# Performance work log

Hardware: AMD Instinct MI355X
Metric: run time of the kernel (lower is better)

## Reference

```python
import jax, jax.numpy as jnp
import numpy as np
from jax.scipy.special import logsumexp

NUM_CLASSES = 2
THRESHOLD = 0.35      # overlap_thresh
NEGPOS_RATIO = 7      # neg_pos
VAR0, VAR1 = 0.1, 0.2  # self.variance


def point_form(p):
    # (cx,cy,w,h) -> (x1,y1,x2,y2)
    return jnp.concatenate([p[:, :2] - p[:, 2:] / 2, p[:, :2] + p[:, 2:] / 2], axis=1)


def jaccard(a, b):
    # a: [T,4] xyxy, b: [P,4] xyxy -> IoU [T,P]
    lt = jnp.maximum(a[:, None, :2], b[None, :, :2])
    rb = jnp.minimum(a[:, None, 2:], b[None, :, 2:])
    wh = jnp.clip(rb - lt, 0.0)
    inter = wh[..., 0] * wh[..., 1]
    area_a = ((a[:, 2] - a[:, 0]) * (a[:, 3] - a[:, 1]))[:, None]
    area_b = ((b[:, 2] - b[:, 0]) * (b[:, 3] - b[:, 1]))[None, :]
    return inter / (area_a + area_b - inter)


def encode(matched, priors):
    # matched xyxy [P,4], priors cxcywh [P,4]
    g_cxcy = ((matched[:, :2] + matched[:, 2:]) / 2 - priors[:, :2]) / (VAR0 * priors[:, 2:])
    g_wh = jnp.log((matched[:, 2:] - matched[:, :2]) / priors[:, 2:]) / VAR1
    return jnp.concatenate([g_cxcy, g_wh], axis=1)


def encode_landm(matched, priors):
    m = matched.reshape(-1, 5, 2)  # [P,5,2]
    g = (m - priors[:, None, :2]) / (VAR0 * priors[:, None, 2:])
    return g.reshape(-1, 10)


def match_one(truths, labels, landms, priors):
    # truths [T,4] xyxy, labels [T], landms [T,10], priors [P,4] cxcywh
    overlaps = jaccard(truths, point_form(priors))  # [T,P]
    best_prior_overlap = overlaps.max(axis=1)       # [T]
    best_prior_idx = overlaps.argmax(axis=1)        # [T]
    valid_gt = best_prior_overlap >= 0.2            # hard-gt filter
    best_truth_overlap = overlaps.max(axis=0)       # [P]
    best_truth_idx = overlaps.argmax(axis=0)        # [P]
    # index_fill_(0, best_prior_idx[valid], 2): IoU <= 1 so scatter-max is exact
    best_truth_overlap = best_truth_overlap.at[best_prior_idx].max(
        jnp.where(valid_gt, 2.0, 0.0))
    best_truth_idx = best_truth_idx.at[best_prior_idx].set(jnp.arange(truths.shape[0]))
    matches = truths[best_truth_idx]                # [P,4]
    conf = jnp.where(best_truth_overlap < THRESHOLD, 0.0, labels[best_truth_idx])
    loc = encode(matches, priors)
    landm = encode_landm(landms[best_truth_idx], priors)
    any_valid = valid_gt.any()                      # early-return branch in torch match()
    loc = jnp.where(any_valid, loc, 0.0)
    conf = jnp.where(any_valid, conf, 0.0)
    landm = jnp.where(any_valid, landm, 0.0)
    return loc, conf.astype(jnp.int32), landm


def smooth_l1(x):
    ax = jnp.abs(x)
    return jnp.where(ax < 1.0, 0.5 * ax * ax, ax - 0.5)


def multibox_loss(loc_data, conf_data, landm_data, priors, targets):
    num_priors = priors.shape[0]
    # torch uses .data (detached) for matching/encoding targets
    truths = jax.lax.stop_gradient(targets[..., :4])
    landms_gt = jax.lax.stop_gradient(targets[..., 4:14])
    labels = jax.lax.stop_gradient(targets[..., 14])
    pri = jax.lax.stop_gradient(priors)
    loc_t, conf_t, landm_t = jax.vmap(match_one, in_axes=(0, 0, 0, None))(
        truths, labels, landms_gt, pri)  # [B,P,4], [B,P], [B,P,10]

    # landmark loss over conf_t > 0
    pos1 = conf_t > 0
    N1 = jnp.maximum(pos1.sum().astype(jnp.float32), 1.0)
    loss_landm = jnp.sum(smooth_l1(landm_data - landm_t) * pos1[..., None])

    # localization loss over conf_t != 0; conf_t[pos] = 1
    pos = conf_t != 0
    conf_t = jnp.where(pos, 1, conf_t)
    loss_l = jnp.sum(smooth_l1(loc_data - loc_t) * pos[..., None])

    # per-prior CE = logsumexp(logits) - logit[target]
    ce = logsumexp(conf_data, axis=-1) - jnp.take_along_axis(
        conf_data, conf_t[..., None], axis=-1)[..., 0]  # [B,P]
    # hard negative mining: zero positives, double-argsort rank trick
    rank_loss = jnp.where(pos, 0.0, ce)
    idx_rank = jnp.argsort(jnp.argsort(-rank_loss, axis=1), axis=1)
    num_pos = pos.sum(axis=1, keepdims=True)
    num_neg = jnp.minimum(NEGPOS_RATIO * num_pos, num_priors - 1)
    neg = idx_rank < num_neg
    loss_c = jnp.sum(jnp.where(pos | neg, ce, 0.0))

    N = jnp.maximum(num_pos.sum().astype(jnp.float32), 1.0)
    return loss_l / N, loss_c / N, loss_landm / N1


def setup_inputs() -> dict:
    key = jax.random.key(0)
    ks = jax.random.split(key, 8)
    B, P, T = 16, 32768, 64
    loc_data = jax.random.normal(ks[0], (B, P, 4), jnp.float32)
    conf_data = jax.random.normal(ks[1], (B, P, NUM_CLASSES), jnp.float32)
    landm_data = jax.random.normal(ks[2], (B, P, 10), jnp.float32)
    # priors: (cx,cy,w,h), all positive and in (0,1)
    cxcy = jax.random.uniform(ks[3], (P, 2), minval=0.05, maxval=0.95)
    wh = jax.random.uniform(ks[4], (P, 2), minval=0.02, maxval=0.3)
    priors = jnp.concatenate([cxcy, wh], axis=1)
    # targets: [x1,y1,x2,y2, 10 landmark coords, label]
    c = jax.random.uniform(ks[5], (B, T, 2), minval=0.15, maxval=0.85)
    s = jax.random.uniform(ks[6], (B, T, 2), minval=0.05, maxval=0.25)
    boxes = jnp.concatenate([c - s / 2, c + s / 2], axis=-1)
    lm = jax.random.uniform(ks[7], (B, T, 10))
    labels = jnp.ones((B, T, 1), jnp.float32)
    targets = jnp.concatenate([boxes, lm, labels], axis=-1)
    return {"loc_data": loc_data, "conf_data": conf_data,
            "landm_data": landm_data, "priors": priors, "targets": targets}


def reference(loc_data, conf_data, landm_data, priors, targets):
    return multibox_loss(loc_data, conf_data, landm_data, priors, targets)
```

## Files before the change

### kernel.cpp

```cpp
#include <hip/hip_runtime.h>
#include <math.h>

#define OVERLAP_THRESH 0.35f
#define VALID_THRESH   0.2f
#define NEGPOS         7
#define TMAX           64
#define NCHUNK         16
#define TPW            4
#define EPT            4
#define HB             2048
#define NC             4
#define NSCAN          32

__device__ __forceinline__ float sl1(float x) {
    float ax = fabsf(x);
    return ax < 1.0f ? 0.5f * ax * ax : ax - 0.5f;
}
__device__ __forceinline__ float frcp(float x) { return __builtin_amdgcn_rcpf(x); }

__device__ __forceinline__ void atomicMaxU8(unsigned char* addr, unsigned char val) {
    size_t a = (size_t)addr;
    unsigned* word = (unsigned*)(a & ~(size_t)3);
    int shift = (int)(a & 3) * 8;
    unsigned old = *word, assumed;
    do {
        unsigned cur = (old >> shift) & 0xFFu;
        if (cur >= val) break;
        assumed = old;
        unsigned nw = (old & ~(0xFFu << shift)) | ((unsigned)val << shift);
        old = atomicCAS(word, assumed, nw);
    } while (old != assumed);
}

__global__ void clear_ws_kernel(uint4* __restrict__ p, size_t n16) {
    size_t i = (size_t)blockIdx.x * blockDim.x + threadIdx.x;
    size_t stride = (size_t)gridDim.x * blockDim.x;
    uint4 z = make_uint4(0u, 0u, 0u, 0u);
    for (; i < n16; i += stride) p[i] = z;
}

__device__ __forceinline__ void select_coarse(const int* gh, int K, int lane,
                                              int* s_d1, int* s_r) {
    int base = lane * 32;
    int v[32]; int s = 0;
    #pragma unroll
    for (int j = 0; j < 32; j++) { v[j] = gh[base + j]; s += v[j]; }
    int sfx = s;
    for (int off = 1; off < 64; off <<= 1) {
        int t = __shfl_down(sfx, off);
        if (lane + off < 64) sfx += t;
    }
    int ge = sfx;
    #pragma unroll
    for (int j = 0; j < 32; j++) {
        int gen = ge - v[j];
        if (ge >= K && gen < K) { *s_d1 = base + j; *s_r = K - gen; }
        ge = gen;
    }
}

__global__ void best_prior_partial_kernel(const float* __restrict__ priors,
                                          const float* __restrict__ targets,
                                          int P, int BT,
                                          unsigned long long* __restrict__ keys) {
    int wid  = blockIdx.x * (blockDim.x >> 6) + (threadIdx.x >> 6);
    int lane = threadIdx.x & 63;
    int ng    = (BT + TPW - 1) / TPW;
    int group = wid % ng;
    int chunk = wid / ng;
    int bt0   = group * TPW;

    float tx1[TPW], ty1[TPW], tx2[TPW], ty2[TPW], ta[TPW];
    #pragma unroll
    for (int j = 0; j < TPW; j++) {
        int bt = min(bt0 + j, BT - 1);
        const float* tg = targets + (size_t)bt * 15;
        tx1[j] = tg[0]; ty1[j] = tg[1]; tx2[j] = tg[2]; ty2[j] = tg[3];
        ta[j]  = (tx2[j] - tx1[j]) * (ty2[j] - ty1[j]);
    }

    int cs = (P + NCHUNK - 1) / NCHUNK;
    int p0 = chunk * cs;
    int pend = min(p0 + cs, P);
    float best[TPW]; int bestp[TPW];
    #pragma unroll
    for (int j = 0; j < TPW; j++) { best[j] = -1.0f; bestp[j] = p0; }

    for (int p = p0 + lane; p < pend; p += 64) {
        float4 pr = ((const float4*)priors)[p];
        float hw = pr.z * 0.5f, hh = pr.w * 0.5f;
        float px1 = pr.x - hw, py1 = pr.y - hh;
        float px2 = pr.x + hw, py2 = pr.y + hh;
        float pa = (px2 - px1) * (py2 - py1);
        #pragma unroll
        for (int j = 0; j < TPW; j++) {
            float iw = fmaxf(fminf(tx2[j], px2) - fmaxf(tx1[j], px1), 0.0f);
            float ih = fmaxf(fminf(ty2[j], py2) - fmaxf(ty1[j], py1), 0.0f);
            float inter = iw * ih;
            float iou = inter * frcp(ta[j] + pa - inter);
            if (iou > best[j]) { best[j] = iou; bestp[j] = p; }
        }
    }
    #pragma unroll
    for (int j = 0; j < TPW; j++) {
        unsigned long long key =
            ((unsigned long long)__float_as_uint(fmaxf(best[j], 0.0f)) << 32) |
            (unsigned long long)(0xFFFFFFFFu - (unsigned)bestp[j]);
        for (int off = 32; off; off >>= 1) {
            unsigned long long k2 = __shfl_down(key, off);
            if (k2 > key) key = k2;
        }
        if (lane == 0 && bt0 + j < BT) atomicMax(&keys[bt0 + j], key);
    }
}

__global__ void unpack_override_kernel(const unsigned long long* __restrict__ keys,
                                       int T, int BT, int P,
                                       unsigned char* __restrict__ ovr8,
                                       unsigned* __restrict__ vmask,
                                       int* __restrict__ av_arr) {
    int i = blockIdx.x * blockDim.x + threadIdx.x;
    if (i >= BT) return;
    unsigned long long k = keys[i];
    int bpi = (int)(0xFFFFFFFFu - (unsigned)(k & 0xFFFFFFFFull));
    float iou = __uint_as_float((unsigned)(k >> 32));
    int b = i / T, t = i % T;
    atomicMaxU8(&ovr8[(size_t)b * P + bpi], (unsigned char)(t + 1));
    if (iou >= VALID_THRESH) {
        atomicOr(&vmask[(size_t)b * (P >> 5) + (bpi >> 5)], 1u << (bpi & 31));
        atomicOr(&av_arr[b], 1);
    }
}

__global__ void match_loss_fused_kernel(const float* __restrict__ priors,
                                        const float* __restrict__ targets,
                                        const float* __restrict__ loc_data,
                                        const float* __restrict__ conf_data,
                                        const float* __restrict__ landm_data,
                                        const unsigned char* __restrict__ ovr8,
                                        const unsigned* __restrict__ vmask,
                                        const int* __restrict__ av_arr,
                                        int P, int T,
                                        float* __restrict__ rank_loss,
                                        int* __restrict__ ghist,
                                        int* __restrict__ num_pos,
                                        int* __restrict__ num_pos1,
                                        float* __restrict__ accb)
{
    int b   = blockIdx.y;
    int tid = threadIdx.x;
    int p0  = (blockIdx.x * blockDim.x + tid) * EPT;
    size_t base = (size_t)b * P + p0;

    __shared__ float4 s_box[TMAX];
    __shared__ float  s_ba[TMAX];
    __shared__ float  s_lab[TMAX];
    __shared__ int    s_hist[HB][NC];
    __shared__ float  s_ll, s_llm, s_cep;
    __shared__ int    s_np, s_np1;

    if (tid == 0) { s_ll = 0.f; s_llm = 0.f; s_cep = 0.f; s_np = 0; s_np1 = 0; }
    for (int i = tid; i < HB; i += blockDim.x)
        *(int4*)&s_hist[i][0] = make_int4(0, 0, 0, 0);
    if (tid < T) {
        const float* tg = targets + ((size_t)b * T + tid) * 15;
        float x1 = tg[0], y1 = tg[1], x2 = tg[2], y2 = tg[3];
        s_box[tid] = make_float4(x1, y1, x2, y2);
        s_ba[tid]  = (x2 - x1) * (y2 - y1);
        s_lab[tid] = tg[14];
    }
    __syncthreads();

    int hc = tid & (NC - 1);
    int av = av_arr[b];
    float ll_s = 0.f, cep_s = 0.f, llm_s = 0.f;
    int np_s = 0, np1_s = 0;

    if (p0 + EPT <= P) {
        float px1[EPT], py1[EPT], px2[EPT], py2[EPT], pa[EPT];
        float pcx[EPT], pcy[EPT], pw[EPT], ph[EPT];
        float best[EPT]; int btidx[EPT];
        #pragma unroll
        for (int j = 0; j < EPT; j++) {
            float4 pr = ((const float4*)priors)[p0 + j];
            float hw = pr.z * 0.5f, hh = pr.w * 0.5f;
            px1[j] = pr.x - hw; py1[j] = pr.y - hh;
            px2[j] = pr.x + hw; py2[j] = pr.y + hh;
            pa[j]  = (px2[j] - px1[j]) * (py2[j] - py1[j]);
            pcx[j] = pr.x; pcy[j] = pr.y; pw[j] = pr.z; ph[j] = pr.w;
            best[j] = -1.0f; btidx[j] = 0;
        }

        #pragma unroll 8
        for (int t = 0; t < TMAX; t++) {
            float4 box = s_box[t];
            float  ba  = s_ba[t];
            #pragma unroll
            for (int j = 0; j < EPT; j++) {
                float iw = fmaxf(fminf(box.z, px2[j]) - fmaxf(box.x, px1[j]), 0.0f);
                float ih = fmaxf(fminf(box.w, py2[j]) - fmaxf(box.y, py1[j]), 0.0f);
                float inter = iw * ih;
                float iou = inter * frcp(ba + pa[j] - inter);
                if (iou > best[j]) { best[j] = iou; btidx[j] = t; }
            }
        }

        unsigned ov4 = *(const unsigned*)&ovr8[base];
        unsigned vb  = vmask[(size_t)b * (P >> 5) + (p0 >> 5)] >> (p0 & 31);
        float cc[2 * EPT];
        *(float4*)&cc[0] = ((const float4*)(conf_data + base * 2))[0];
        *(float4*)&cc[4] = ((const float4*)(conf_data + base * 2))[1];

        float rl[EPT]; int btv[EPT]; float cev[EPT]; int posv[EPT];
        #pragma unroll
        for (int j = 0; j < EPT; j++) {
            int bt = btidx[j];
            int ov = (ov4 >> (8 * j)) & 0xFF;
            if (ov) bt = ov - 1;
            float bv = best[j];
            if ((vb >> j) & 1u) bv = 2.0f;
            btv[j] = bt;

            bool cond = (av && bv >= OVERLAP_THRESH);
            float lab = cond ? s_lab[bt] : 0.0f;
            int   ci  = (int)lab;
            bool  pos = cond && (ci != 0);
            posv[j] = pos;

            float c0 = cc[2 * j], c1 = cc[2 * j + 1];
            float mx = fmaxf(c0, c1);
            float lse = mx + __logf(1.0f + __expf(-fabsf(c0 - c1)));
            float ce  = lse - (pos ? c1 : c0);
            cev[j] = ce;
            rl[j] = pos ? 0.0f : fmaxf(ce, 0.0f);
            atomicAdd(&s_hist[__float_as_uint(rl[j]) >> 20][hc], 1);
        }
        *(float4*)&rank_loss[base] = *(float4*)rl;

        #pragma unroll
        for (int j = 0; j < EPT; j++) {
            if (!posv[j]) continue;
            int bt = btv[j];
            size_t idx = base + j;
            float4 mb = s_box[bt];
            bool pos1 = ((int)s_lab[bt] > 0);

            float rx = frcp(0.1f * pw[j]), ry = frcp(0.1f * ph[j]);
            float gx = ((mb.x + mb.z) * 0.5f - pcx[j]) * rx;
            float gy = ((mb.y + mb.w) * 0.5f - pcy[j]) * ry;
            float gw = __logf((mb.z - mb.x) * frcp(pw[j])) * 5.0f;
            float gh = __logf((mb.w - mb.y) * frcp(ph[j])) * 5.0f;
            const float* ld = loc_data + idx * 4;
            ll_s += sl1(ld[0] - gx) + sl1(ld[1] - gy) + sl1(ld[2] - gw) + sl1(ld[3] - gh);
            cep_s += cev[j];
            np_s++;

            if (pos1) {
                const float* lmd = landm_data + idx * 10;
                const float* lm  = targets + ((size_t)b * T + bt) * 15 + 4;
                float s = 0.0f;
                #pragma unroll
                for (int k = 0; k < 5; k++) {
                    float gxl = (lm[2 * k]     - pcx[j]) * rx;
                    float gyl = (lm[2 * k + 1] - pcy[j]) * ry;
                    s += sl1(lmd[2 * k] - gxl) + sl1(lmd[2 * k + 1] - gyl);
                }
                llm_s += s;
                np1_s++;
            }
        }
    }

    if (np_s)  { atomicAdd(&s_ll, ll_s); atomicAdd(&s_cep, cep_s); atomicAdd(&s_np, np_s); }
    if (np1_s) { atomicAdd(&s_llm, llm_s); atomicAdd(&s_np1, np1_s); }
    __syncthreads();
    if (tid == 0) {
        if (s_np)  { atomicAdd(&num_pos[b], s_np);
                     atomicAdd(&accb[b * 3 + 0], s_ll);
                     atomicAdd(&accb[b * 3 + 2], s_cep); }
        if (s_np1) { atomicAdd(&num_pos1[b], s_np1);
                     atomicAdd(&accb[b * 3 + 1], s_llm); }
    }
    for (int i = tid; i < HB; i += blockDim.x) {
        int4 v4 = *(int4*)&s_hist[i][0];
        int v = v4.x + v4.y + v4.z + v4.w;
        if (v) atomicAdd(&ghist[(size_t)b * HB + i], v);
    }
}

__device__ __forceinline__ void select_digit(const int* hist, int nb, int tid,
                                             int* s_dig, int* s_r) {
    if (tid < 64) {
        int lane = tid;
        int per  = (nb >= 64) ? (nb >> 6) : 1;
        int base = lane * per;
        int v[4]; int s = 0;
        #pragma unroll
        for (int j = 0; j < 4; j++) {
            int idx = base + j;
            int h = (j < per && idx < nb) ? hist[idx] : 0;
            v[j] = h; s += h;
        }
        int sfx = s;
        for (int off = 1; off < 64; off <<= 1) {
            int t = __shfl_down(sfx, off);
            if (lane + off < 64) sfx += t;
        }
        int r  = *s_r;
        int ge = sfx;
        #pragma unroll
        for (int j = 0; j < 4; j++) {
            int gen = ge - v[j];
            int d   = base + j;
            if (j < per && d < nb && ge >= r && gen < r) { *s_dig = d; *s_r = r - gen; }
            ge = gen;
        }
    }
}

__global__ void topk_scan_kernel(const float* __restrict__ rank_loss,
                                 const int* __restrict__ num_pos,
                                 const int* __restrict__ ghist,
                                 int P,
                                 float* __restrict__ glist,
                                 int* __restrict__ gcnt,
                                 float* __restrict__ accS,
                                 int* __restrict__ accC) {
    int b    = blockIdx.y;
    int tid  = threadIdx.x;
    int lane = tid & 63;
    int wv   = tid >> 6;
    long long Kll = (long long)num_pos[b] * NEGPOS;
    int K = (Kll > P - 1) ? (P - 1) : (int)Kll;
    if (K <= 0) return;

    __shared__ int   s_d1, s_rdummy;
    __shared__ int   s_lcnt, s_base;
    __shared__ float s_stage[1024];
    __shared__ float s_S[4];
    __shared__ int   s_C[4];

    if (tid == 0) s_lcnt = 0;
    if (wv == 0) select_coarse(ghist + (size_t)b * HB, K, lane, &s_d1, &s_rdummy);
    __syncthreads();
    int d1 = s_d1;
    unsigned hi_lim = ((unsigned)(d1 + 1)) << 20;

    const float4* v4 = (const float4*)(rank_loss + (size_t)b * P);
    int n4  = P >> 2;
    int per = (n4 + NSCAN - 1) / NSCAN;
    int i0  = blockIdx.x * per;
    int i1  = min(i0 + per, n4);

    float S = 0.f; int C = 0;
    if (d1 == 0) {
        for (int i = i0 + tid; i < i1; i += blockDim.x) {
            float4 x = v4[i];
            float xs[4] = {x.x, x.y, x.z, x.w};
            #pragma unroll
            for (int k = 0; k < 4; k++) {
                unsigned u = __float_as_uint(xs[k]);
                if (u >= hi_lim) { S += xs[k]; C++; }
            }
        }
    } else {
        for (int i = i0 + tid; i < i1; i += blockDim.x) {
            float4 x = v4[i];
            float xs[4] = {x.x, x.y, x.z, x.w};
            #pragma unroll
            for (int k = 0; k < 4; k++) {
                unsigned u = __float_as_uint(xs[k]);
                if (u >= hi_lim) { S += xs[k]; C++; }
                bool m = ((u >> 20) == (unsigned)d1);
                unsigned long long mk = __ballot(m);
                if (m) {
                    int leader = __ffsll((long long)mk) - 1;
                    int base = 0;
                    if (lane == leader) base = atomicAdd(&s_lcnt, __popcll(mk));
                    base = __shfl(base, leader);
                    int ofs = __popcll(mk & (((unsigned long long)1 << lane) - 1ull));
                    s_stage[base + ofs] = xs[k];
                }
            }
        }
    }
    for (int off = 32; off; off >>= 1) {
        S += __shfl_down(S, off);
        C += __shfl_down(C, off);
    }
    if (lane == 0) { s_S[wv] = S; s_C[wv] = C; }
    __syncthreads();
    if (tid == 0) {
        float St = 0.f; int Ct = 0;
        for (int i = 0; i < 4; i++) { St += s_S[i]; Ct += s_C[i]; }
        if (Ct) { atomicAdd(&accS[b], St); atomicAdd(&accC[b], Ct); }
        s_base = s_lcnt ? atomicAdd(&gcnt[b], s_lcnt) : 0;
    }
    __syncthreads();
    int lc = s_lcnt, gbase = s_base;
    float* gl = glist + (size_t)b * P;
    for (int i = tid; i < lc; i += blockDim.x) gl[gbase + i] = s_stage[i];
}

__global__ void topk_refine_finalize_kernel(const int* __restrict__ num_pos,
                                            const int* __restrict__ num_pos1,
                                            const float* __restrict__ accb,
                                            const int* __restrict__ ghist,
                                            int P, int B,
                                            const float* __restrict__ glist,
                                            const int* __restrict__ gcnt,
                                            const float* __restrict__ accS,
                                            const int* __restrict__ accC,
                                            float* __restrict__ accn,
                                            int* __restrict__ done_ctr,
                                            float* __restrict__ out) {
    int b    = blockIdx.x;
    int tid  = threadIdx.x;
    int lane = tid & 63;
    int wv   = tid >> 6;
    long long Kll = (long long)num_pos[b] * NEGPOS;
    int K = (Kll > P - 1) ? (P - 1) : (int)Kll;

    __shared__ int   hist[256];
    __shared__ int   s_d1, s_r, s_dig;
    __shared__ float s_S[16];
    __shared__ int   s_C[16];
    __shared__ float s_res;

    if (tid == 0) s_res = 0.0f;
    __syncthreads();

    if (K > 0) {
        if (wv == 0) select_coarse(ghist + (size_t)b * HB, K, lane, &s_d1, &s_r);
        __syncthreads();
        int d1 = s_d1;

        if (d1 == 0) {
            if (tid == 0) s_res = accS[b];
            __syncthreads();
        } else {
            int lc = gcnt[b];
            const float* gl = glist + (size_t)b * P;

            unsigned pmask = 0u, pval = 0u;
            const int shf[3] = {12, 4, 0};
            const int nbk[3] = {256, 256, 16};
            int trips = (lc + blockDim.x - 1) / blockDim.x;
            for (int ps = 0; ps < 3; ps++) {
                int sh = shf[ps]; unsigned wm = (unsigned)(nbk[ps] - 1);
                if (tid < 256) hist[tid] = 0;
                __syncthreads();
                for (int tc = 0; tc < trips; tc++) {
                    int i = tc * blockDim.x + tid;
                    bool ok = (i < lc);
                    unsigned u = ok ? __float_as_uint(gl[i]) : 0u;
                    ok = ok && ((u & pmask) == pval);
                    unsigned d = (u >> sh) & wm;
                    unsigned long long m = __ballot(ok);
                    #pragma unroll
                    for (int bit = 0; bit < 8; bit++) {
                        unsigned long long bb = __ballot((d >> bit) & 1u);
                        m &= ((d >> bit) & 1u) ? bb : ~bb;
                    }
                    if (ok && lane == (__ffsll((long long)m) - 1))
                        atomicAdd(&hist[d], __popcll(m));
                }
                __syncthreads();
                select_digit(hist, nbk[ps], tid, &s_dig, &s_r);
                __syncthreads();
                pval  |= ((unsigned)s_dig) << sh;
                pmask |= wm << sh;
            }
            float tau = __uint_as_float((((unsigned)d1) << 20) | pval);

            float S = 0.f; int C = 0;
            for (int i = tid; i < lc; i += blockDim.x) {
                float x = gl[i];
                if (x > tau) { S += x; C++; }
            }
            for (int off = 32; off; off >>= 1) {
                S += __shfl_down(S, off);
                C += __shfl_down(C, off);
            }
            if (lane == 0) { s_S[wv] = S; s_C[wv] = C; }
            __syncthreads();
            if (tid == 0) {
                float St = accS[b]; int Ct = accC[b];
                int nw = blockDim.x >> 6;
                for (int i = 0; i < nw; i++) { St += s_S[i]; Ct += s_C[i]; }
                s_res = St + (float)(K - Ct) * tau;
            }
            __syncthreads();
        }
    }

    if (tid == 0) {
        accn[b] = s_res;
        __threadfence();
        if (atomicAdd(done_ctr, 1) == B - 1) {
            float cen = 0.f;
            for (int j = 0; j < B; j++) cen += atomicAdd(&accn[j], 0.0f);
            int tp = 0, tp1 = 0;
            float ll = 0.f, llm = 0.f, cep = 0.f;
            for (int j = 0; j < B; j++) {
                tp  += num_pos[j];
                tp1 += num_pos1[j];
                ll  += accb[j * 3 + 0];
                llm += accb[j * 3 + 1];
                cep += accb[j * 3 + 2];
            }
            float N  = fmaxf((float)tp, 1.0f);
            float N1 = fmaxf((float)tp1, 1.0f);
            out[0] = ll / N;
            out[1] = (cep + cen) / N;
            out[2] = llm / N1;
        }
    }
}

extern "C" void kernel_launch(void* const* d_in, const int* in_sizes, int n_in,
                              void* d_out, int out_size, void* d_ws, size_t ws_size,
                              hipStream_t stream) {
    const float* loc_data   = (const float*)d_in[0];
    const float* conf_data  = (const float*)d_in[1];
    const float* landm_data = (const float*)d_in[2];
    const float* priors     = (const float*)d_in[3];
    const float* targets    = (const float*)d_in[4];
    float* out = (float*)d_out;

    int P  = in_sizes[3] / 4;
    int BP = in_sizes[0] / 4;
    int B  = BP / P;
    int T  = in_sizes[4] / (B * 15);
    int BT = B * T;

    char* ws = (char*)d_ws;
    float* rank_loss = (float*)ws;                    size_t off = (size_t)B * P * sizeof(float);
    float* glist     = (float*)(ws + off);            off += (size_t)B * P * sizeof(float);
    unsigned char* ovr8 = (unsigned char*)(ws + off); off += (size_t)B * P;
    unsigned* vmask = (unsigned*)(ws + off); off += (size_t)B * (P >> 5) * sizeof(unsigned);
    int* ghist      = (int*)(ws + off);      off += (size_t)B * HB * sizeof(int);
    unsigned long long* keys = (unsigned long long*)(ws + off); off += (size_t)BT * sizeof(unsigned long long);
    int* av_arr     = (int*)(ws + off);      off += (size_t)B * sizeof(int);
    int* num_pos    = (int*)(ws + off);      off += (size_t)B * sizeof(int);
    int* num_pos1   = (int*)(ws + off);      off += (size_t)B * sizeof(int);
    float* accb     = (float*)(ws + off);    off += (size_t)B * 3 * sizeof(float);
    float* accn     = (float*)(ws + off);    off += (size_t)B * sizeof(float);
    int* gcnt       = (int*)(ws + off);      off += (size_t)B * sizeof(int);
    float* accS     = (float*)(ws + off);    off += (size_t)B * sizeof(float);
    int* accC       = (int*)(ws + off);      off += (size_t)B * sizeof(int);
    int* done_ctr   = (int*)(ws + off);      off += sizeof(int);

    size_t zbytes = (size_t)((char*)(done_ctr + 1) - (char*)ovr8);
    size_t n16 = (zbytes + 15) / 16;
    clear_ws_kernel<<<256, 256, 0, stream>>>((uint4*)ovr8, n16);

    int waves   = NCHUNK * ((BT + TPW - 1) / TPW);
    int blocks2 = (waves + 3) / 4;
    best_prior_partial_kernel<<<blocks2, 256, 0, stream>>>(priors, targets, P, BT, keys);

    unpack_override_kernel<<<(BT + 255) / 256, 256, 0, stream>>>(keys, T, BT, P,
                                                                 ovr8, vmask, av_arr);

    dim3 gm((P + 256 * EPT - 1) / (256 * EPT), B);
    match_loss_fused_kernel<<<gm, 256, 0, stream>>>(priors, targets, loc_data, conf_data,
                                                    landm_data, ovr8, vmask, av_arr, P, T,
                                                    rank_loss, ghist, num_pos, num_pos1, accb);

    dim3 gs(NSCAN, B);
    topk_scan_kernel<<<gs, 256, 0, stream>>>(rank_loss, num_pos, ghist, P,
                                             glist, gcnt, accS, accC);

    topk_refine_finalize_kernel<<<B, 1024, 0, stream>>>(num_pos, num_pos1, accb, ghist,
                                                        P, B, glist, gcnt, accS, accC,
                                                        accn, done_ctr, out);
}
```

Baseline: 104.5 us.

## Fuse best-prior search with override unpack; skip positives in histogram

Replaces the chunked best-prior kernel plus the global 64-bit atomicMax keys buffer and separate unpack kernel with one kernel. Each block now scans all priors for four targets and reduces the result in shared memory, then writes the override, valid mask and any-valid flags directly. This removes one launch and the global atomics. Separately, positive priors are no longer added to the rank-loss histogram, and their count is added back to bin 0 in select_coarse, which cuts shared atomics. The trade-off is that each block now walks the full prior range, so there are fewer blocks with longer loops.

```diff
diff --git a/kernel.cpp b/kernel.cpp
--- a/kernel.cpp
+++ b/kernel.cpp
@@ -5,8 +5,7 @@
 #define VALID_THRESH   0.2f
 #define NEGPOS         7
 #define TMAX           64
-#define NCHUNK         16
-#define TPW            4
+#define TPB2           4
 #define EPT            4
 #define HB             2048
 #define NC             4
@@ -39,12 +38,16 @@
     for (; i < n16; i += stride) p[i] = z;
 }
 
-__device__ __forceinline__ void select_coarse(const int* gh, int K, int lane,
+__device__ __forceinline__ void select_coarse(const int* gh, int K, int lane, int add0,
                                               int* s_d1, int* s_r) {
     int base = lane * 32;
     int v[32]; int s = 0;
     #pragma unroll
-    for (int j = 0; j < 32; j++) { v[j] = gh[base + j]; s += v[j]; }
+    for (int j = 0; j < 32; j++) {
+        int h = gh[base + j];
+        if (base + j == 0) h += add0;
+        v[j] = h; s += h;
+    }
     int sfx = s;
     for (int off = 1; off < 64; off <<= 1) {
         int t = __shfl_down(sfx, off);
@@ -59,41 +62,38 @@
     }
 }
 
-__global__ void best_prior_partial_kernel(const float* __restrict__ priors,
-                                          const float* __restrict__ targets,
-                                          int P, int BT,
-                                          unsigned long long* __restrict__ keys) {
-    int wid  = blockIdx.x * (blockDim.x >> 6) + (threadIdx.x >> 6);
-    int lane = threadIdx.x & 63;
-    int ng    = (BT + TPW - 1) / TPW;
-    int group = wid % ng;
-    int chunk = wid / ng;
-    int bt0   = group * TPW;
-
-    float tx1[TPW], ty1[TPW], tx2[TPW], ty2[TPW], ta[TPW];
+__global__ void best_prior_fused_kernel(const float* __restrict__ priors,
+                                        const float* __restrict__ targets,
+                                        int P, int T, int BT,
+                                        unsigned char* __restrict__ ovr8,
+                                        unsigned* __restrict__ vmask,
+                                        int* __restrict__ av_arr) {
+    int tid  = threadIdx.x;
+    int lane = tid & 63;
+    int wv   = tid >> 6;
+    int bt0  = blockIdx.x * TPB2;
+
+    float tx1[TPB2], ty1[TPB2], tx2[TPB2], ty2[TPB2], ta[TPB2];
     #pragma unroll
-    for (int j = 0; j < TPW; j++) {
+    for (int j = 0; j < TPB2; j++) {
         int bt = min(bt0 + j, BT - 1);
         const float* tg = targets + (size_t)bt * 15;
         tx1[j] = tg[0]; ty1[j] = tg[1]; tx2[j] = tg[2]; ty2[j] = tg[3];
         ta[j]  = (tx2[j] - tx1[j]) * (ty2[j] - ty1[j]);
     }
 
-    int cs = (P + NCHUNK - 1) / NCHUNK;
-    int p0 = chunk * cs;
-    int pend = min(p0 + cs, P);
-    float best[TPW]; int bestp[TPW];
+    float best[TPB2]; int bestp[TPB2];
     #pragma unroll
-    for (int j = 0; j < TPW; j++) { best[j] = -1.0f; bestp[j] = p0; }
-
-    for (int p = p0 + lane; p < pend; p += 64) {
+    for (int j = 0; j < TPB2; j++) { best[j] = -1.0f; bestp[j] = 0; }
+
+    for (int p = tid; p < P; p += 256) {
         float4 pr = ((const float4*)priors)[p];
         float hw = pr.z * 0.5f, hh = pr.w * 0.5f;
         float px1 = pr.x - hw, py1 = pr.y - hh;
         float px2 = pr.x + hw, py2 = pr.y + hh;
         float pa = (px2 - px1) * (py2 - py1);
         #pragma unroll
-        for (int j = 0; j < TPW; j++) {
+        for (int j = 0; j < TPB2; j++) {
             float iw = fmaxf(fminf(tx2[j], px2) - fmaxf(tx1[j], px1), 0.0f);
             float ih = fmaxf(fminf(ty2[j], py2) - fmaxf(ty1[j], py1), 0.0f);
             float inter = iw * ih;
@@ -101,8 +101,10 @@
             if (iou > best[j]) { best[j] = iou; bestp[j] = p; }
         }
     }
+
+    __shared__ unsigned long long s_red[TPB2][4];
     #pragma unroll
-    for (int j = 0; j < TPW; j++) {
+    for (int j = 0; j < TPB2; j++) {
         unsigned long long key =
             ((unsigned long long)__float_as_uint(fmaxf(best[j], 0.0f)) << 32) |
             (unsigned long long)(0xFFFFFFFFu - (unsigned)bestp[j]);
@@ -110,25 +112,24 @@
             unsigned long long k2 = __shfl_down(key, off);
             if (k2 > key) key = k2;
         }
-        if (lane == 0 && bt0 + j < BT) atomicMax(&keys[bt0 + j], key);
-    }
-}
-
-__global__ void unpack_override_kernel(const unsigned long long* __restrict__ keys,
-                                       int T, int BT, int P,
-                                       unsigned char* __restrict__ ovr8,
-                                       unsigned* __restrict__ vmask,
-                                       int* __restrict__ av_arr) {
-    int i = blockIdx.x * blockDim.x + threadIdx.x;
-    if (i >= BT) return;
-    unsigned long long k = keys[i];
-    int bpi = (int)(0xFFFFFFFFu - (unsigned)(k & 0xFFFFFFFFull));
-    float iou = __uint_as_float((unsigned)(k >> 32));
-    int b = i / T, t = i % T;
-    atomicMaxU8(&ovr8[(size_t)b * P + bpi], (unsigned char)(t + 1));
-    if (iou >= VALID_THRESH) {
-        atomicOr(&vmask[(size_t)b * (P >> 5) + (bpi >> 5)], 1u << (bpi & 31));
-        atomicOr(&av_arr[b], 1);
+        if (lane == 0) s_red[j][wv] = key;
+    }
+    __syncthreads();
+    if (tid < TPB2) {
+        unsigned long long k = s_red[tid][0];
+        #pragma unroll
+        for (int w = 1; w < 4; w++) if (s_red[tid][w] > k) k = s_red[tid][w];
+        int bt = bt0 + tid;
+        if (bt < BT) {
+            int bpi = (int)(0xFFFFFFFFu - (unsigned)(k & 0xFFFFFFFFull));
+            float iou = __uint_as_float((unsigned)(k >> 32));
+            int b = bt / T, t = bt % T;
+            atomicMaxU8(&ovr8[(size_t)b * P + bpi], (unsigned char)(t + 1));
+            if (iou >= VALID_THRESH) {
+                atomicOr(&vmask[(size_t)b * (P >> 5) + (bpi >> 5)], 1u << (bpi & 31));
+                atomicOr(&av_arr[b], 1);
+            }
+        }
     }
 }
 
@@ -233,7 +234,7 @@
             float ce  = lse - (pos ? c1 : c0);
             cev[j] = ce;
             rl[j] = pos ? 0.0f : fmaxf(ce, 0.0f);
-            atomicAdd(&s_hist[__float_as_uint(rl[j]) >> 20][hc], 1);
+            if (!pos) atomicAdd(&s_hist[__float_as_uint(rl[j]) >> 20][hc], 1);
         }
         *(float4*)&rank_loss[base] = *(float4*)rl;
 
@@ -330,7 +331,8 @@
     int tid  = threadIdx.x;
     int lane = tid & 63;
     int wv   = tid >> 6;
-    long long Kll = (long long)num_pos[b] * NEGPOS;
+    int np   = num_pos[b];
+    long long Kll = (long long)np * NEGPOS;
     int K = (Kll > P - 1) ? (P - 1) : (int)Kll;
     if (K <= 0) return;
 
@@ -341,7 +343,7 @@
     __shared__ int   s_C[4];
 
     if (tid == 0) s_lcnt = 0;
-    if (wv == 0) select_coarse(ghist + (size_t)b * HB, K, lane, &s_d1, &s_rdummy);
+    if (wv == 0) select_coarse(ghist + (size_t)b * HB, K, lane, np, &s_d1, &s_rdummy);
     __syncthreads();
     int d1 = s_d1;
     unsigned hi_lim = ((unsigned)(d1 + 1)) << 20;
@@ -418,7 +420,8 @@
     int tid  = threadIdx.x;
     int lane = tid & 63;
     int wv   = tid >> 6;
-    long long Kll = (long long)num_pos[b] * NEGPOS;
+    int np   = num_pos[b];
+    long long Kll = (long long)np * NEGPOS;
     int K = (Kll > P - 1) ? (P - 1) : (int)Kll;
 
     __shared__ int   hist[256];
@@ -431,7 +434,7 @@
     __syncthreads();
 
     if (K > 0) {
-        if (wv == 0) select_coarse(ghist + (size_t)b * HB, K, lane, &s_d1, &s_r);
+        if (wv == 0) select_coarse(ghist + (size_t)b * HB, K, lane, np, &s_d1, &s_r);
         __syncthreads();
         int d1 = s_d1;
 
@@ -540,7 +543,6 @@
     unsigned char* ovr8 = (unsigned char*)(ws + off); off += (size_t)B * P;
     unsigned* vmask = (unsigned*)(ws + off); off += (size_t)B * (P >> 5) * sizeof(unsigned);
     int* ghist      = (int*)(ws + off);      off += (size_t)B * HB * sizeof(int);
-    unsigned long long* keys = (unsigned long long*)(ws + off); off += (size_t)BT * sizeof(unsigned long long);
     int* av_arr     = (int*)(ws + off);      off += (size_t)B * sizeof(int);
     int* num_pos    = (int*)(ws + off);      off += (size_t)B * sizeof(int);
     int* num_pos1   = (int*)(ws + off);      off += (size_t)B * sizeof(int);
@@ -555,12 +557,9 @@
     size_t n16 = (zbytes + 15) / 16;
     clear_ws_kernel<<<256, 256, 0, stream>>>((uint4*)ovr8, n16);
 
-    int waves   = NCHUNK * ((BT + TPW - 1) / TPW);
-    int blocks2 = (waves + 3) / 4;
-    best_prior_partial_kernel<<<blocks2, 256, 0, stream>>>(priors, targets, P, BT, keys);
-
-    unpack_override_kernel<<<(BT + 255) / 256, 256, 0, stream>>>(keys, T, BT, P,
-                                                                 ovr8, vmask, av_arr);
+    int blocks2 = (BT + TPB2 - 1) / TPB2;
+    best_prior_fused_kernel<<<blocks2, 256, 0, stream>>>(priors, targets, P, T, BT,
+                                                         ovr8, vmask, av_arr);
 
     dim3 gm((P + 256 * EPT - 1) / (256 * EPT), B);
     match_loss_fused_kernel<<<gm, 256, 0, stream>>>(priors, targets, loc_data, conf_data,
```

Result: slower. 128.4 us (+22.8%).
